# Kernel optimization log

Measured on AMD Instinct MI355X. Metric: run time of the kernel, lower is better.

Reference implementation:

```python
import jax, jax.numpy as jnp
import numpy as np

P = 0.3
SHAPE = (8192, 4096)
SIZE = SHAPE[0] * SHAPE[1]
K = int(SIZE * P)


def setup_inputs() -> dict:
    key = jax.random.key(0)
    kx, ki = jax.random.split(key)
    X = jax.random.normal(kx, SHAPE, dtype=jnp.float32)
    # without-replacement sample of K flat indices (mirrors np.random.choice(replace=False));
    # duplicates would be harmless anyway since the op is set-to-zero.
    drop_idx = jnp.asarray(np.random.default_rng(0).permutation(SIZE)[:K], dtype=jnp.int64)
    return {"X": X, "drop_idx": drop_idx}


def reference(X, drop_idx):
    # zero exactly the chosen flat positions, no 1/(1-p) rescale (faithful to source)
    out = X.reshape(-1).at[drop_idx].set(0.0).reshape(X.shape)
    return out
```

## Files before the change

kernel.cpp:

```cpp
#include <hip/hip_runtime.h>
#include <stdint.h>

#define THREADS 256

typedef float __attribute__((ext_vector_type(4))) fvec4;

#define RB2 15
#define HREGION 32768u
#define NHB 1024
#define ATILE 16384
#define CAPH 24
#define OSTAGE 128
#define BTHREADS 512
#define MAXTILES 768
#define CELLQ (CAPH / 8)
#define TILEQ (NHB * CELLQ)

__global__ __launch_bounds__(BTHREADS)
void bin_sent_kernel(const int* __restrict__ idx, int k, int ntiles,
                     uint16_t* __restrict__ bdata,
                     uint32_t* __restrict__ ovf_tcnt, uint32_t* __restrict__ ovf) {
    __shared__ uint16_t stage[NHB * CAPH];
    __shared__ uint32_t lcnt[NHB];
    __shared__ uint32_t ostage[OSTAGE];
    __shared__ uint32_t ocnt_l;
    const int t = blockIdx.x;

    uint4* st4 = (uint4*)stage;
    for (int j = threadIdx.x; j < (int)(NHB * CAPH * 2 / 16); j += BTHREADS)
        st4[j] = make_uint4(~0u, ~0u, ~0u, ~0u);
    for (int b = threadIdx.x; b < NHB; b += BTHREADS) lcnt[b] = 0u;
    if (threadIdx.x == 0) ocnt_l = 0u;
    __syncthreads();

    const int base = t * ATILE;
    const int lim = (k - base < ATILE) ? (k - base) : ATILE;
    if (lim == ATILE) {
        const int4* idx4 = (const int4*)(idx + base);
        for (int j = threadIdx.x; j < ATILE / 4; j += BTHREADS) {
            const int4 v4 = idx4[j];
            const int vs[4] = {v4.x, v4.y, v4.z, v4.w};
            #pragma unroll
            for (int e = 0; e < 4; ++e) {
                const unsigned v = (unsigned)vs[e];
                const unsigned b = v >> RB2;
                const unsigned off = v & 0x7FFFu;
                const unsigned lp = atomicAdd(&lcnt[b], 1u);
                if (lp < CAPH) stage[b * CAPH + lp] = (uint16_t)off;
                else {
                    const unsigned o = atomicAdd(&ocnt_l, 1u);
                    if (o < OSTAGE) ostage[o] = v;
                }
            }
        }
    } else {
        for (int j = threadIdx.x; j < lim; j += BTHREADS) {
            const unsigned v = (unsigned)idx[base + j];
            const unsigned b = v >> RB2;
            const unsigned off = v & 0x7FFFu;
            const unsigned lp = atomicAdd(&lcnt[b], 1u);
            if (lp < CAPH) stage[b * CAPH + lp] = (uint16_t)off;
            else {
                const unsigned o = atomicAdd(&ocnt_l, 1u);
                if (o < OSTAGE) ostage[o] = v;
            }
        }
    }
    __syncthreads();

    {
        unsigned m = ocnt_l;
        if (m > OSTAGE) m = OSTAGE;
        if (threadIdx.x == 0) ovf_tcnt[t] = m;
        for (unsigned j = threadIdx.x; j < m; j += BTHREADS)
            ovf[(size_t)t * OSTAGE + j] = ostage[j];
    }
    uint4* bd4 = (uint4*)(bdata + (size_t)t * NHB * CAPH);
    for (int j = threadIdx.x; j < (int)TILEQ; j += BTHREADS)
        bd4[j] = st4[j];
}

__global__ __launch_bounds__(512)
void apply_sent_kernel(const float* __restrict__ Xs, float* __restrict__ outs,
                       int ntiles, const uint16_t* __restrict__ bdata) {
    __shared__ uint8_t lmask[HREGION];
    const int hr = blockIdx.x;

    uint4* lm4 = (uint4*)lmask;
    for (int j = threadIdx.x; j < (int)(HREGION / 16); j += 512)
        lm4[j] = make_uint4(0u, 0u, 0u, 0u);
    __syncthreads();

    const uint4* bd4 = (const uint4*)bdata;
    const int nq = ntiles * CELLQ;
    for (int i = threadIdx.x; i < nq; i += 512) {
        const int t = i / CELLQ;
        const int q = i - t * CELLQ;
        const uint4 w4 = bd4[(size_t)t * TILEQ + (size_t)hr * CELLQ + q];
        const unsigned ws[4] = {w4.x, w4.y, w4.z, w4.w};
        #pragma unroll
        for (int e = 0; e < 4; ++e) {
            const unsigned e0 = ws[e] & 0xFFFFu;
            const unsigned e1 = ws[e] >> 16;
            if (e0 < 0x8000u) lmask[e0] = (uint8_t)1;
            if (e1 < 0x8000u) lmask[e1] = (uint8_t)1;
        }
    }
    __syncthreads();

    const uint32_t* lm32 = (const uint32_t*)lmask;
    const fvec4* X4 = (const fvec4*)Xs;
    fvec4* out4 = (fvec4*)outs;
    const int base4 = (int)((unsigned)hr << 13);
    for (int j = threadIdx.x; j < (int)(HREGION / 4); j += 512) {
        const int g = base4 + j;
        fvec4 v = X4[g];
        const uint32_t mm = lm32[j];
        if (mm & 0x000000FFu) v.x = 0.0f;
        if (mm & 0x0000FF00u) v.y = 0.0f;
        if (mm & 0x00FF0000u) v.z = 0.0f;
        if (mm & 0xFF000000u) v.w = 0.0f;
        __builtin_nontemporal_store(v, &out4[g]);
    }
}

__global__ void ovf_tile_scatter_kernel(const uint32_t* __restrict__ ovf_tcnt,
                                        const uint32_t* __restrict__ ovf,
                                        float* __restrict__ out) {
    const int t = blockIdx.x;
    unsigned m = ovf_tcnt[t];
    if (m > OSTAGE) m = OSTAGE;
    for (unsigned j = threadIdx.x; j < m; j += blockDim.x)
        out[ovf[(size_t)t * OSTAGE + j]] = 0.0f;
}


__global__ void zero_mask4_kernel(uint4* __restrict__ mask, int nquads) {
    int i = blockIdx.x * blockDim.x + threadIdx.x;
    int stride = gridDim.x * blockDim.x;
    uint4 z = make_uint4(0u, 0u, 0u, 0u);
    for (; i < nquads; i += stride) mask[i] = z;
}

__global__ void scatter_bytes_kernel(const int* __restrict__ idx, int k,
                                     uint8_t* __restrict__ mask) {
    int i = blockIdx.x * blockDim.x + threadIdx.x;
    int stride = gridDim.x * blockDim.x;
    for (; i < k; i += stride) mask[(unsigned)idx[i]] = (uint8_t)1;
}

__global__ void apply_bytes_kernel(const float4* __restrict__ X,
                                   const uint32_t* __restrict__ maskw,
                                   float4* __restrict__ out, int nvec) {
    int i = blockIdx.x * blockDim.x + threadIdx.x;
    int stride = gridDim.x * blockDim.x;
    for (int j = i; j < nvec; j += stride) {
        float4 v = X[j];
        uint32_t m = maskw[j];
        if (m & 0x000000FFu) v.x = 0.0f;
        if (m & 0x0000FF00u) v.y = 0.0f;
        if (m & 0x00FF0000u) v.z = 0.0f;
        if (m & 0xFF000000u) v.w = 0.0f;
        out[j] = v;
    }
}


__global__ void copy_kernel(const float4* __restrict__ X, float4* __restrict__ out,
                            int nvec) {
    int i = blockIdx.x * blockDim.x + threadIdx.x;
    int stride = gridDim.x * blockDim.x;
    for (int j = i; j < nvec; j += stride) out[j] = X[j];
}

__global__ void scatter_zero_kernel(const int* __restrict__ idx, int k,
                                    float* __restrict__ out) {
    int i = blockIdx.x * blockDim.x + threadIdx.x;
    int stride = gridDim.x * blockDim.x;
    for (; i < k; i += stride) out[idx[i]] = 0.0f;
}

extern "C" void kernel_launch(void* const* d_in, const int* in_sizes, int n_in,
                              void* d_out, int out_size, void* d_ws, size_t ws_size,
                              hipStream_t stream) {
    const float* X = (const float*)d_in[0];
    const int* drop_idx = (const int*)d_in[1];
    float* out = (float*)d_out;

    const int n = out_size;
    const int k = in_sizes[1];
    const int nvec = n >> 2;

    if ((unsigned)n == NHB * HREGION && k > 0) {
        const int ntiles = (k + ATILE - 1) / ATILE;
        const size_t bdata_bytes = (size_t)NHB * ntiles * CAPH * 2;
        const size_t tcnt_bytes = (size_t)ntiles * 4;
        const size_t ovf_bytes = (size_t)ntiles * OSTAGE * 4;
        const size_t need = bdata_bytes + tcnt_bytes + ovf_bytes + 64;
        if (ntiles <= MAXTILES && ws_size >= need) {
            uint16_t* bdata = (uint16_t*)d_ws;
            uint32_t* ovf_tcnt = (uint32_t*)((char*)d_ws + bdata_bytes);
            uint32_t* ovf = (uint32_t*)((char*)d_ws + bdata_bytes + tcnt_bytes);

            bin_sent_kernel<<<ntiles, BTHREADS, 0, stream>>>(
                drop_idx, k, ntiles, bdata, ovf_tcnt, ovf);
            apply_sent_kernel<<<NHB, 512, 0, stream>>>(
                X, out, ntiles, bdata);
            ovf_tile_scatter_kernel<<<ntiles, 64, 0, stream>>>(ovf_tcnt, ovf, out);
            return;
        }
    }

    if (ws_size >= (size_t)n && (n & 15) == 0) {
        uint8_t* mask = (uint8_t*)d_ws;
        zero_mask4_kernel<<<2048, THREADS, 0, stream>>>((uint4*)mask, n >> 4);
        scatter_bytes_kernel<<<2048, THREADS, 0, stream>>>(drop_idx, k, mask);
        apply_bytes_kernel<<<2048, THREADS, 0, stream>>>(
            (const float4*)X, (const uint32_t*)mask, (float4*)out, nvec);
        return;
    }

    copy_kernel<<<2048, THREADS, 0, stream>>>((const float4*)X, (float4*)out, nvec);
    scatter_zero_kernel<<<2048, THREADS, 0, stream>>>(drop_idx, k, out);
}
```

Baseline: 80.17 us.

## Transpose bin storage to cell-major and pack per-bin counters into halfwords

Bins are now stored cell-major, so each apply block reads one contiguous run of all tiles' entries for its region. Before, each block gathered scattered 16-byte chunks from every tile. Tile size and per-cell capacity shrink (16 slots per cell, smaller tiles, larger overflow stage), and the shared counters are packed two per 32-bit word to save LDS. The smaller tiles mean more bin blocks and more overflow traffic, and the bin kernel's global writes are now strided.

```diff
diff --git a/kernel.cpp b/kernel.cpp
--- a/kernel.cpp
+++ b/kernel.cpp
@@ -8,20 +8,18 @@
 #define RB2 15
 #define HREGION 32768u
 #define NHB 1024
-#define ATILE 16384
-#define CAPH 24
-#define OSTAGE 128
+#define ATILE 10920
+#define CAPH 16
+#define OSTAGE 256
 #define BTHREADS 512
-#define MAXTILES 768
-#define CELLQ (CAPH / 8)
-#define TILEQ (NHB * CELLQ)
+#define MAXTILES 1100
 
 __global__ __launch_bounds__(BTHREADS)
 void bin_sent_kernel(const int* __restrict__ idx, int k, int ntiles,
                      uint16_t* __restrict__ bdata,
                      uint32_t* __restrict__ ovf_tcnt, uint32_t* __restrict__ ovf) {
     __shared__ uint16_t stage[NHB * CAPH];
-    __shared__ uint32_t lcnt[NHB];
+    __shared__ uint32_t lcntp[NHB / 2];
     __shared__ uint32_t ostage[OSTAGE];
     __shared__ uint32_t ocnt_l;
     const int t = blockIdx.x;
@@ -29,7 +27,7 @@
     uint4* st4 = (uint4*)stage;
     for (int j = threadIdx.x; j < (int)(NHB * CAPH * 2 / 16); j += BTHREADS)
         st4[j] = make_uint4(~0u, ~0u, ~0u, ~0u);
-    for (int b = threadIdx.x; b < NHB; b += BTHREADS) lcnt[b] = 0u;
+    for (int b = threadIdx.x; b < NHB / 2; b += BTHREADS) lcntp[b] = 0u;
     if (threadIdx.x == 0) ocnt_l = 0u;
     __syncthreads();
 
@@ -45,7 +43,9 @@
                 const unsigned v = (unsigned)vs[e];
                 const unsigned b = v >> RB2;
                 const unsigned off = v & 0x7FFFu;
-                const unsigned lp = atomicAdd(&lcnt[b], 1u);
+                const unsigned sh = (b & 1u) << 4;
+                const unsigned old = atomicAdd(&lcntp[b >> 1], 1u << sh);
+                const unsigned lp = (old >> sh) & 0xFFFFu;
                 if (lp < CAPH) stage[b * CAPH + lp] = (uint16_t)off;
                 else {
                     const unsigned o = atomicAdd(&ocnt_l, 1u);
@@ -58,7 +58,9 @@
             const unsigned v = (unsigned)idx[base + j];
             const unsigned b = v >> RB2;
             const unsigned off = v & 0x7FFFu;
-            const unsigned lp = atomicAdd(&lcnt[b], 1u);
+            const unsigned sh = (b & 1u) << 4;
+            const unsigned old = atomicAdd(&lcntp[b >> 1], 1u << sh);
+            const unsigned lp = (old >> sh) & 0xFFFFu;
             if (lp < CAPH) stage[b * CAPH + lp] = (uint16_t)off;
             else {
                 const unsigned o = atomicAdd(&ocnt_l, 1u);
@@ -75,9 +77,12 @@
         for (unsigned j = threadIdx.x; j < m; j += BTHREADS)
             ovf[(size_t)t * OSTAGE + j] = ostage[j];
     }
-    uint4* bd4 = (uint4*)(bdata + (size_t)t * NHB * CAPH);
-    for (int j = threadIdx.x; j < (int)TILEQ; j += BTHREADS)
-        bd4[j] = st4[j];
+    uint4* bd4 = (uint4*)bdata;
+    for (int j = threadIdx.x; j < (int)(NHB * 2); j += BTHREADS) {
+        const int c = j >> 1;
+        const int q = j & 1;
+        bd4[((size_t)c * ntiles + t) * 2 + q] = st4[j];
+    }
 }
 
 __global__ __launch_bounds__(512)
@@ -91,12 +96,10 @@
         lm4[j] = make_uint4(0u, 0u, 0u, 0u);
     __syncthreads();
 
-    const uint4* bd4 = (const uint4*)bdata;
-    const int nq = ntiles * CELLQ;
+    const uint4* bd4 = (const uint4*)(bdata + (size_t)hr * ntiles * CAPH);
+    const int nq = ntiles * 2;
     for (int i = threadIdx.x; i < nq; i += 512) {
-        const int t = i / CELLQ;
-        const int q = i - t * CELLQ;
-        const uint4 w4 = bd4[(size_t)t * TILEQ + (size_t)hr * CELLQ + q];
+        const uint4 w4 = bd4[i];
         const unsigned ws[4] = {w4.x, w4.y, w4.z, w4.w};
         #pragma unroll
         for (int e = 0; e < 4; ++e) {
```

Result: faster. 73.52 us (-8.3%).
